# Kernel tuning notes

Measured on AMD Instinct MI355X. Metric: run time of the kernel, lower is better.

Reference implementation:

```python
import jax, jax.numpy as jnp
import numpy as np

N_QUBITS = 6
N_LAYERS = 3
FEATURE_DIM = 512
ENC_HIDDEN = max(32, N_QUBITS * 4)  # 32
HEAD_HIDDEN = 128
G, T = 54, 24
DIM = 2 ** N_QUBITS  # 64


def _ry_batched(angles):
    # angles: [B] -> batched RY matrices [B, 2, 2] (complex64)
    c = jnp.cos(angles * 0.5)
    s = jnp.sin(angles * 0.5)
    U = jnp.stack([jnp.stack([c, -s], -1), jnp.stack([s, c], -1)], -2)
    return U.astype(jnp.complex64)


def _rot(phi, theta, omega):
    # PennyLane Rot = RZ(omega) RY(theta) RZ(phi); returns [2, 2] complex64
    c = jnp.cos(theta * 0.5).astype(jnp.complex64)
    s = jnp.sin(theta * 0.5).astype(jnp.complex64)
    ep = jnp.exp(-0.5j * (phi + omega).astype(jnp.complex64))  # e^{-i(phi+omega)/2}
    em = jnp.exp(-0.5j * (phi - omega).astype(jnp.complex64))  # e^{-i(phi-omega)/2}
    u00 = ep * c
    u01 = -jnp.conj(em) * s
    u10 = em * s
    u11 = jnp.conj(ep) * c
    return jnp.stack([jnp.stack([u00, u01]), jnp.stack([u10, u11])])


def _apply_1q_batched(state, U, q):
    # state: [B, 2^n]; U: [B, 2, 2] (per-sample gate, e.g. data-encoding RY)
    B = state.shape[0]
    st = state.reshape(B, 2 ** q, 2, -1)
    st = jnp.einsum('bij,bljr->blir', U, st)
    return st.reshape(B, -1)


def _apply_1q(state, U, q):
    # state: [B, 2^n]; U: [2, 2] shared across batch (trainable Rot)
    B = state.shape[0]
    st = state.reshape(B, 2 ** q, 2, -1)
    st = jnp.einsum('ij,bljr->blir', U, st)
    return st.reshape(B, -1)


def _apply_cnot(state, c, t):
    # state: [B, 2^n]; flip target axis where control bit == 1
    B = state.shape[0]
    st = state.reshape((B,) + (2,) * N_QUBITS)
    ax_c, ax_t = 1 + c, 1 + t
    s0 = jnp.take(st, 0, axis=ax_c)
    s1 = jnp.take(st, 1, axis=ax_c)
    s1 = jnp.flip(s1, axis=ax_t if ax_t < ax_c else ax_t - 1)
    st = jnp.stack([s0, s1], axis=ax_c)
    return st.reshape(B, -1)


def _expvals_z(state):
    # <Z_q> for every qubit: [B, n]
    B = state.shape[0]
    probs = (state.real ** 2 + state.imag ** 2).reshape((B,) + (2,) * N_QUBITS)
    outs = []
    for q in range(N_QUBITS):
        axes = tuple(i for i in range(1, N_QUBITS + 1) if i != q + 1)
        p = probs.sum(axes)  # [B, 2]
        outs.append(p[:, 0] - p[:, 1])
    return jnp.stack(outs, -1)


def _circuit(angles, q_weights):
    # angles: [B, n_qubits] float32; q_weights: [L, n, 3]
    B = angles.shape[0]
    state = jnp.zeros((B, DIM), jnp.complex64).at[:, 0].set(1.0)
    for layer in range(N_LAYERS):
        # data_reuploading=True -> re-encode every layer
        for q in range(N_QUBITS):
            state = _apply_1q_batched(state, _ry_batched(angles[:, q]), q)
        for q in range(N_QUBITS):
            w = q_weights[layer, q]
            state = _apply_1q(state, _rot(w[0], w[1], w[2]), q)
        for q in range(0, N_QUBITS - 1, 2):
            state = _apply_cnot(state, q, q + 1)
        for q in range(1, N_QUBITS - 1, 2):
            state = _apply_cnot(state, q, q + 1)
        state = _apply_cnot(state, N_QUBITS - 1, 0)  # n_qubits > 2
    return _expvals_z(state)


def setup_inputs() -> dict:
    key = jax.random.key(0)
    ks = jax.random.split(key, 10)
    B = 32768
    return {
        'x': jax.random.normal(ks[0], (B, FEATURE_DIM), jnp.float32),
        'enc_w1': 0.05 * jax.random.normal(ks[1], (FEATURE_DIM, ENC_HIDDEN), jnp.float32),
        'enc_b1': jnp.zeros((ENC_HIDDEN,), jnp.float32),
        'enc_w2': 0.05 * jax.random.normal(ks[2], (ENC_HIDDEN, N_QUBITS), jnp.float32),
        'enc_b2': jnp.zeros((N_QUBITS,), jnp.float32),
        'q_weights': 0.01 * jax.random.normal(ks[3], (N_LAYERS, N_QUBITS, 3), jnp.float32),
        'head_w1': 0.1 * jax.random.normal(ks[4], (N_QUBITS, HEAD_HIDDEN), jnp.float32),
        'head_b1': jnp.zeros((HEAD_HIDDEN,), jnp.float32),
        'head_w2': 0.05 * jax.random.normal(ks[5], (HEAD_HIDDEN, G * T), jnp.float32),
        'head_b2': jnp.zeros((G * T,), jnp.float32),
    }


def reference(x, enc_w1, enc_b1, enc_w2, enc_b2, q_weights,
              head_w1, head_b1, head_w2, head_b2):
    # classical encoder -> angles [B, n_qubits]
    h = jnp.tanh(x @ enc_w1 + enc_b1)
    angles = h @ enc_w2 + enc_b2
    # batched state-vector PQC simulation
    z = _circuit(angles, q_weights).astype(jnp.float32)  # [B, n_qubits]
    # classical head (dropout is identity in eval)
    g = jax.nn.relu(z @ head_w1 + head_b1)
    logits = g @ head_w2 + head_b2
    return logits.reshape(-1, G, T)
```

## Files before the change

### kernel.cpp

```cpp
#include <hip/hip_runtime.h>

typedef __bf16 bf16x8 __attribute__((ext_vector_type(8)));
typedef float floatx4 __attribute__((ext_vector_type(4)));
typedef unsigned short ushort8 __attribute__((ext_vector_type(8)));

__device__ __forceinline__ unsigned short f2bf(float f) {
    unsigned u = __float_as_uint(f);
    u += 0x7fffu + ((u >> 16) & 1u);
    return (unsigned short)(u >> 16);
}

template <int ST>
__device__ __forceinline__ void apply_local(float* fr, float* fi,
    float m00r, float m00i, float m01r, float m01i,
    float m10r, float m10i, float m11r, float m11i) {
#pragma unroll
    for (int i = 0; i < 8; ++i) {
        if ((i & ST) == 0) {
            int i1 = i + ST;
            float r0 = fr[i], u0 = fi[i], r1 = fr[i1], u1 = fi[i1];
            fr[i]  = m00r * r0 - m00i * u0 + m01r * r1 - m01i * u1;
            fi[i]  = m00r * u0 + m00i * r0 + m01r * u1 + m01i * r1;
            fr[i1] = m10r * r0 - m10i * u0 + m11r * r1 - m11i * u1;
            fi[i1] = m10r * u0 + m10i * r0 + m11r * u1 + m11i * r1;
        }
    }
}

template <int XM>
__device__ __forceinline__ void apply_cross(float* fr, float* fi, bool hi,
    float m00r, float m00i, float m01r, float m01i,
    float m10r, float m10i, float m11r, float m11i) {
    float car = hi ? m10r : m00r, cai = hi ? m10i : m00i;
    float cbr = hi ? m11r : m01r, cbi = hi ? m11i : m01i;
#pragma unroll
    for (int j = 0; j < 8; ++j) {
        float mr = fr[j], mi = fi[j];
        float pr = __shfl_xor(mr, XM);
        float pi = __shfl_xor(mi, XM);
        float a0r = hi ? pr : mr, a0i = hi ? pi : mi;
        float a1r = hi ? mr : pr, a1i = hi ? mi : pi;
        fr[j] = car * a0r - cai * a0i + cbr * a1r - cbi * a1i;
        fi[j] = car * a0i + cai * a0r + cbr * a1i + cbi * a1r;
    }
}

#define SWAP2(a, b) { float _t = fr[a]; fr[a] = fr[b]; fr[b] = _t; \
                      _t = fi[a]; fi[a] = fi[b]; fi[b] = _t; }

__global__ __launch_bounds__(512) void prep_kernel(
    const float* __restrict__ hw2, unsigned short* __restrict__ w2t) {
    int t = blockIdx.x * 512 + threadIdx.x;
    int nn = t >> 4;
    int kc = (t & 15) * 8;
    if (nn < 1296) {
        ushort8 pk;
#pragma unroll
        for (int j = 0; j < 8; ++j) pk[j] = f2bf(hw2[(size_t)(kc + j) * 1296 + nn]);
        *(ushort8*)(w2t + (size_t)nn * 128 + kc) = pk;
    }
}

__global__ __launch_bounds__(512, 4) void front_kernel(
    const float* __restrict__ x, const float* __restrict__ w1,
    const float* __restrict__ b1, const float* __restrict__ w2,
    const float* __restrict__ b2, const float* __restrict__ qw,
    const float* __restrict__ hw1, const float* __restrict__ hb1,
    unsigned short* __restrict__ g) {

    __shared__ float part[8][64][33];
    __shared__ float umat_s[144];

    float (*hsh)[33] = part[0];
    float (*casa)[12] = (float (*)[12])part[1];

    int tid = threadIdx.x;

    if (tid < 18) {
        float phi = qw[tid * 3], theta = qw[tid * 3 + 1], omega = qw[tid * 3 + 2];
        float c = cosf(0.5f * theta), s = sinf(0.5f * theta);
        float po = 0.5f * (phi + omega), pm = 0.5f * (phi - omega);
        float epr = cosf(po), epi = -sinf(po);
        float emr = cosf(pm), emi = -sinf(pm);
        float* u = umat_s + tid * 8;
        u[0] = epr * c;  u[1] = epi * c;
        u[2] = -emr * s; u[3] = emi * s;
        u[4] = emr * s;  u[5] = emi * s;
        u[6] = epr * c;  u[7] = -epi * c;
    }

    int lane = tid & 63;
    int wave = tid >> 6;
    int swave = __builtin_amdgcn_readfirstlane(wave);
    size_t row = (size_t)blockIdx.x * 64 + lane;
    const float2* x2 = (const float2*)(x + row * 512 + swave * 64);
    const float* wseg = w1 + swave * 64 * 32;

    float acc[32];
#pragma unroll
    for (int j = 0; j < 32; ++j) acc[j] = 0.f;

#pragma clang loop unroll(disable)
    for (int k2 = 0; k2 < 32; ++k2) {
        float2 xv = x2[k2];
        const float* wr = wseg + k2 * 64;
#pragma unroll
        for (int j = 0; j < 32; ++j) acc[j] = fmaf(wr[j], xv.x, acc[j]);
#pragma unroll
        for (int j = 0; j < 32; ++j) acc[j] = fmaf(wr[32 + j], xv.y, acc[j]);
    }
#pragma unroll
    for (int j = 0; j < 32; ++j) part[wave][lane][j] = acc[j];
    __syncthreads();

    {
        int rl = tid & 63;
        int jg = (tid >> 6) * 4;
#pragma unroll
        for (int jj = 0; jj < 4; ++jj) {
            int j = jg + jj;
            float v = b1[j];
#pragma unroll
            for (int w = 0; w < 8; ++w) v += part[w][rl][j];
            hsh[rl][j] = tanhf(v);
        }
    }
    __syncthreads();

    if (tid < 384) {
        int row_a = tid & 63;
        int q = tid >> 6;
        float a = b2[q];
#pragma unroll
        for (int j = 0; j < 32; ++j) a = fmaf(hsh[row_a][j], w2[j * 6 + q], a);
        a *= 0.5f;
        casa[row_a][q * 2]     = cosf(a);
        casa[row_a][q * 2 + 1] = sinf(a);
    }
    __syncthreads();

    int s8 = lane & 7;
    int p = lane >> 3;
    int samp = wave * 8 + s8;
    bool pb4 = (p & 4) != 0, pb2 = (p & 2) != 0, pb1 = (p & 1) != 0;

    float ca[6], sa[6];
#pragma unroll
    for (int q = 0; q < 6; ++q) { ca[q] = casa[samp][q * 2]; sa[q] = casa[samp][q * 2 + 1]; }

    float fr[8], fi[8];
#pragma unroll
    for (int j = 0; j < 8; ++j) { fr[j] = 0.f; fi[j] = 0.f; }
    fr[0] = (p == 0) ? 1.f : 0.f;

#pragma clang loop unroll(disable)
    for (int layer = 0; layer < 3; ++layer) {
        const float* ub = umat_s + layer * 48;
#define MAT(Q)                                                            \
        const float* u = ub + (Q) * 8;                                    \
        float c = ca[Q], ss = sa[Q];                                      \
        float m00r = u[0] * c + u[2] * ss, m00i = u[1] * c + u[3] * ss;   \
        float m01r = u[2] * c - u[0] * ss, m01i = u[3] * c - u[1] * ss;   \
        float m10r = u[4] * c + u[6] * ss, m10i = u[5] * c + u[7] * ss;   \
        float m11r = u[6] * c - u[4] * ss, m11i = u[7] * c - u[5] * ss;
        { MAT(0) apply_cross<32>(fr, fi, pb4, m00r, m00i, m01r, m01i, m10r, m10i, m11r, m11i); }
        { MAT(1) apply_cross<16>(fr, fi, pb2, m00r, m00i, m01r, m01i, m10r, m10i, m11r, m11i); }
        { MAT(2) apply_cross<8>(fr, fi, pb1, m00r, m00i, m01r, m01i, m10r, m10i, m11r, m11i); }
        { MAT(3) apply_local<4>(fr, fi, m00r, m00i, m01r, m01i, m10r, m10i, m11r, m11i); }
        { MAT(4) apply_local<2>(fr, fi, m00r, m00i, m01r, m01i, m10r, m10i, m11r, m11i); }
        { MAT(5) apply_local<1>(fr, fi, m00r, m00i, m01r, m01i, m10r, m10i, m11r, m11i); }
#undef MAT
#pragma unroll
        for (int j = 0; j < 8; ++j) {
            float pr = __shfl_xor(fr[j], 16);
            float pi = __shfl_xor(fi[j], 16);
            fr[j] = pb4 ? pr : fr[j];
            fi[j] = pb4 ? pi : fi[j];
        }
        {
            float tr[8], ti[8];
#pragma unroll
            for (int j = 0; j < 8; ++j) { tr[j] = fr[j]; ti[j] = fi[j]; }
#pragma unroll
            for (int j = 0; j < 8; ++j) {
                fr[j] = pb1 ? tr[j ^ 4] : tr[j];
                fi[j] = pb1 ? ti[j ^ 4] : ti[j];
            }
        }
        SWAP2(2, 3) SWAP2(6, 7)
#pragma unroll
        for (int j = 0; j < 8; ++j) {
            float pr = __shfl_xor(fr[j], 8);
            float pi = __shfl_xor(fi[j], 8);
            fr[j] = pb2 ? pr : fr[j];
            fi[j] = pb2 ? pi : fi[j];
        }
        SWAP2(4, 6) SWAP2(5, 7)
#pragma unroll
        for (int j = 1; j < 8; j += 2) {
            fr[j] = __shfl_xor(fr[j], 32);
            fi[j] = __shfl_xor(fi[j], 32);
        }
    }

    float zt = 0.f, z3 = 0.f, z4 = 0.f, z5 = 0.f;
#pragma unroll
    for (int j = 0; j < 8; ++j) {
        float pp = fr[j] * fr[j] + fi[j] * fi[j];
        zt += pp;
        z3 += (j & 4) ? -pp : pp;
        z4 += (j & 2) ? -pp : pp;
        z5 += (j & 1) ? -pp : pp;
    }
    float zz[6];
    zz[0] = pb4 ? -zt : zt;
    zz[1] = pb2 ? -zt : zt;
    zz[2] = pb1 ? -zt : zt;
    zz[3] = z3; zz[4] = z4; zz[5] = z5;
#pragma unroll
    for (int q = 0; q < 6; ++q) {
        zz[q] += __shfl_xor(zz[q], 8);
        zz[q] += __shfl_xor(zz[q], 16);
        zz[q] += __shfl_xor(zz[q], 32);
    }

    {
        unsigned short* gp = g + ((size_t)blockIdx.x * 64 + samp) * 128 + p * 16;
#pragma unroll
        for (int half = 0; half < 2; ++half) {
            ushort8 pk;
#pragma unroll
            for (int jj = 0; jj < 8; ++jj) {
                int j = p * 16 + half * 8 + jj;
                float a = hb1[j];
#pragma unroll
                for (int q = 0; q < 6; ++q) a = fmaf(zz[q], hw1[q * 128 + j], a);
                a = fmaxf(a, 0.f);
                pk[jj] = f2bf(a);
            }
            *(ushort8*)(gp + half * 8) = pk;
        }
    }
}

__global__ __launch_bounds__(256) void head_gemm(
    const unsigned short* __restrict__ g, const unsigned short* __restrict__ w2t,
    const float* __restrict__ b2, float* __restrict__ out) {
    __shared__ unsigned short gl[16 * 128];

    int tid = threadIdx.x;
    int row0 = blockIdx.x * 16;

    {
        int r = tid >> 4;
        int u = tid & 15;
        ushort8 v = *(const ushort8*)(g + (size_t)(row0 + r) * 128 + u * 8);
        int us = u ^ (r & 7);
        *(ushort8*)(gl + r * 128 + us * 8) = v;
    }
    __syncthreads();

    int lane = tid & 63, wv = tid >> 6;
    int l15 = lane & 15, quad = lane >> 4;
    int a7 = l15 & 7;

    for (int n = wv; n < 27; n += 4) {
        int col0 = n * 48;
#pragma unroll
        for (int t = 0; t < 3; ++t) {
            const unsigned short* ap =
                w2t + (size_t)(col0 + t * 16 + l15) * 128 + quad * 8;

            floatx4 acc = (floatx4)0.f;
#pragma unroll
            for (int ks = 0; ks < 4; ++ks) {
                bf16x8 af = *(const bf16x8*)(ap + ks * 32);
                int u = (quad + 4 * ks) ^ a7;
                bf16x8 bf = *(const bf16x8*)(gl + l15 * 128 + u * 8);
                acc = __builtin_amdgcn_mfma_f32_16x16x32_bf16(af, bf, acc, 0, 0, 0);
            }

            const float* bb = b2 + col0 + t * 16 + quad * 4;
            floatx4 bias = { bb[0], bb[1], bb[2], bb[3] };
            floatx4 v = acc + bias;
            *(floatx4*)(out + (size_t)(row0 + l15) * 1296 + col0 + t * 16 + quad * 4) = v;
        }
    }
}

extern "C" void kernel_launch(void* const* d_in, const int* in_sizes, int n_in,
                              void* d_out, int out_size, void* d_ws, size_t ws_size,
                              hipStream_t stream) {
    const float* x   = (const float*)d_in[0];
    const float* ew1 = (const float*)d_in[1];
    const float* eb1 = (const float*)d_in[2];
    const float* ew2 = (const float*)d_in[3];
    const float* eb2 = (const float*)d_in[4];
    const float* qw  = (const float*)d_in[5];
    const float* hw1 = (const float*)d_in[6];
    const float* hb1 = (const float*)d_in[7];
    const float* hw2 = (const float*)d_in[8];
    const float* hb2 = (const float*)d_in[9];
    float* out = (float*)d_out;

    char* ws = (char*)d_ws;
    unsigned short* g   = (unsigned short*)(ws);
    unsigned short* w2t = (unsigned short*)(ws + 8388608);

    prep_kernel<<<dim3(41), dim3(512), 0, stream>>>(hw2, w2t);
    front_kernel<<<dim3(512), dim3(512), 0, stream>>>(
        x, ew1, eb1, ew2, eb2, qw, hw1, hb1, g);
    head_gemm<<<dim3(2048), dim3(256), 0, stream>>>(g, w2t, hb2, out);
}
```

Baseline: 370.9 us.

## Split front kernel into encoder and circuit kernels; fuse head layer-1 into GEMM

Splits the monolithic front kernel into an encoder kernel (256 threads, 4 waves each covering 128 input features) that writes angles, and a separate circuit kernel that computes cos/sin and runs the state-vector simulation, writing only 6 expectation values per sample. Rot-matrix setup moves into the prep kernel. The head's first layer (z @ hw1 + relu, bf16 pack) moves into the head GEMM prologue, so the 128-wide g intermediate is no longer written to or read from global memory. The cost is an extra kernel launch and small angles/z round trips, plus lower encoder parallelism per row.

```diff
diff --git a/kernel.cpp b/kernel.cpp
--- a/kernel.cpp
+++ b/kernel.cpp
@@ -49,8 +49,21 @@
                       _t = fi[a]; fi[a] = fi[b]; fi[b] = _t; }
 
 __global__ __launch_bounds__(512) void prep_kernel(
-    const float* __restrict__ hw2, unsigned short* __restrict__ w2t) {
+    const float* __restrict__ hw2, const float* __restrict__ qw,
+    unsigned short* __restrict__ w2t, float* __restrict__ umat) {
     int t = blockIdx.x * 512 + threadIdx.x;
+    if (t < 18) {
+        float phi = qw[t * 3], theta = qw[t * 3 + 1], omega = qw[t * 3 + 2];
+        float c = cosf(0.5f * theta), s = sinf(0.5f * theta);
+        float po = 0.5f * (phi + omega), pm = 0.5f * (phi - omega);
+        float epr = cosf(po), epi = -sinf(po);
+        float emr = cosf(pm), emi = -sinf(pm);
+        float* u = umat + t * 8;
+        u[0] = epr * c;  u[1] = epi * c;
+        u[2] = -emr * s; u[3] = emi * s;
+        u[4] = emr * s;  u[5] = emi * s;
+        u[6] = epr * c;  u[7] = -epi * c;
+    }
     int nn = t >> 4;
     int kc = (t & 15) * 8;
     if (nn < 1296) {
@@ -61,47 +74,25 @@
     }
 }
 
-__global__ __launch_bounds__(512, 4) void front_kernel(
+__global__ __launch_bounds__(256) void enc_kernel(
     const float* __restrict__ x, const float* __restrict__ w1,
     const float* __restrict__ b1, const float* __restrict__ w2,
-    const float* __restrict__ b2, const float* __restrict__ qw,
-    const float* __restrict__ hw1, const float* __restrict__ hb1,
-    unsigned short* __restrict__ g) {
-
-    __shared__ float part[8][64][33];
-    __shared__ float umat_s[144];
-
-    float (*hsh)[33] = part[0];
-    float (*casa)[12] = (float (*)[12])part[1];
-
-    int tid = threadIdx.x;
-
-    if (tid < 18) {
-        float phi = qw[tid * 3], theta = qw[tid * 3 + 1], omega = qw[tid * 3 + 2];
-        float c = cosf(0.5f * theta), s = sinf(0.5f * theta);
-        float po = 0.5f * (phi + omega), pm = 0.5f * (phi - omega);
-        float epr = cosf(po), epi = -sinf(po);
-        float emr = cosf(pm), emi = -sinf(pm);
-        float* u = umat_s + tid * 8;
-        u[0] = epr * c;  u[1] = epi * c;
-        u[2] = -emr * s; u[3] = emi * s;
-        u[4] = emr * s;  u[5] = emi * s;
-        u[6] = epr * c;  u[7] = -epi * c;
-    }
-
-    int lane = tid & 63;
-    int wave = tid >> 6;
+    const float* __restrict__ b2, float* __restrict__ angles) {
+    __shared__ float part[4][64][33];
+    __shared__ float hsh[64][33];
+    int lane = threadIdx.x & 63;
+    int wave = threadIdx.x >> 6;
     int swave = __builtin_amdgcn_readfirstlane(wave);
     size_t row = (size_t)blockIdx.x * 64 + lane;
-    const float2* x2 = (const float2*)(x + row * 512 + swave * 64);
-    const float* wseg = w1 + swave * 64 * 32;
+    const float2* x2 = (const float2*)(x + row * 512 + swave * 128);
+    const float* wseg = w1 + swave * 128 * 32;
 
     float acc[32];
 #pragma unroll
     for (int j = 0; j < 32; ++j) acc[j] = 0.f;
 
 #pragma clang loop unroll(disable)
-    for (int k2 = 0; k2 < 32; ++k2) {
+    for (int k2 = 0; k2 < 64; ++k2) {
         float2 xv = x2[k2];
         const float* wr = wseg + k2 * 64;
 #pragma unroll
@@ -113,40 +104,48 @@
     for (int j = 0; j < 32; ++j) part[wave][lane][j] = acc[j];
     __syncthreads();
 
-    {
-        int rl = tid & 63;
-        int jg = (tid >> 6) * 4;
-#pragma unroll
-        for (int jj = 0; jj < 4; ++jj) {
-            int j = jg + jj;
-            float v = b1[j];
-#pragma unroll
-            for (int w = 0; w < 8; ++w) v += part[w][rl][j];
-            hsh[rl][j] = tanhf(v);
-        }
+    int rl = threadIdx.x & 63;
+    int jg = (threadIdx.x >> 6) * 8;
+#pragma unroll
+    for (int jj = 0; jj < 8; ++jj) {
+        int j = jg + jj;
+        float v = part[0][rl][j] + part[1][rl][j] + part[2][rl][j] + part[3][rl][j] + b1[j];
+        hsh[rl][j] = tanhf(v);
     }
     __syncthreads();
 
-    if (tid < 384) {
-        int row_a = tid & 63;
-        int q = tid >> 6;
-        float a = b2[q];
-#pragma unroll
-        for (int j = 0; j < 32; ++j) a = fmaf(hsh[row_a][j], w2[j * 6 + q], a);
-        a *= 0.5f;
-        casa[row_a][q * 2]     = cosf(a);
-        casa[row_a][q * 2 + 1] = sinf(a);
-    }
-    __syncthreads();
-
+    if (threadIdx.x < 64) {
+        float h[32];
+#pragma unroll
+        for (int j = 0; j < 32; ++j) h[j] = hsh[threadIdx.x][j];
+#pragma unroll
+        for (int q = 0; q < 6; ++q) {
+            float a = b2[q];
+#pragma unroll
+            for (int j = 0; j < 32; ++j) a = fmaf(h[j], w2[j * 6 + q], a);
+            angles[((size_t)blockIdx.x * 64 + threadIdx.x) * 6 + q] = a;
+        }
+    }
+}
+
+__global__ __launch_bounds__(256) void circuit_kernel(
+    const float* __restrict__ angles, const float* __restrict__ umat,
+    float* __restrict__ z) {
+    int tid = threadIdx.x;
+    int lane = tid & 63;
+    int wv = tid >> 6;
     int s8 = lane & 7;
     int p = lane >> 3;
-    int samp = wave * 8 + s8;
+    int samp = blockIdx.x * 32 + wv * 8 + s8;
     bool pb4 = (p & 4) != 0, pb2 = (p & 2) != 0, pb1 = (p & 1) != 0;
 
     float ca[6], sa[6];
 #pragma unroll
-    for (int q = 0; q < 6; ++q) { ca[q] = casa[samp][q * 2]; sa[q] = casa[samp][q * 2 + 1]; }
+    for (int q = 0; q < 6; ++q) {
+        float a = 0.5f * angles[(size_t)samp * 6 + q];
+        ca[q] = cosf(a);
+        sa[q] = sinf(a);
+    }
 
     float fr[8], fi[8];
 #pragma unroll
@@ -155,7 +154,7 @@
 
 #pragma clang loop unroll(disable)
     for (int layer = 0; layer < 3; ++layer) {
-        const float* ub = umat_s + layer * 48;
+        const float* ub = umat + layer * 48;
 #define MAT(Q)                                                            \
         const float* u = ub + (Q) * 8;                                    \
         float c = ca[Q], ss = sa[Q];                                      \
@@ -223,40 +222,41 @@
         zz[q] += __shfl_xor(zz[q], 16);
         zz[q] += __shfl_xor(zz[q], 32);
     }
-
-    {
-        unsigned short* gp = g + ((size_t)blockIdx.x * 64 + samp) * 128 + p * 16;
-#pragma unroll
-        for (int half = 0; half < 2; ++half) {
-            ushort8 pk;
-#pragma unroll
-            for (int jj = 0; jj < 8; ++jj) {
-                int j = p * 16 + half * 8 + jj;
-                float a = hb1[j];
-#pragma unroll
-                for (int q = 0; q < 6; ++q) a = fmaf(zz[q], hw1[q * 128 + j], a);
-                a = fmaxf(a, 0.f);
-                pk[jj] = f2bf(a);
-            }
-            *(ushort8*)(gp + half * 8) = pk;
-        }
-    }
+    if (p < 6) z[(size_t)samp * 6 + p] = zz[p];
 }
 
 __global__ __launch_bounds__(256) void head_gemm(
-    const unsigned short* __restrict__ g, const unsigned short* __restrict__ w2t,
+    const float* __restrict__ z, const unsigned short* __restrict__ w2t,
+    const float* __restrict__ hw1, const float* __restrict__ hb1,
     const float* __restrict__ b2, float* __restrict__ out) {
     __shared__ unsigned short gl[16 * 128];
+    __shared__ float zsh[16][6];
 
     int tid = threadIdx.x;
     int row0 = blockIdx.x * 16;
+
+    if (tid < 96) zsh[tid / 6][tid % 6] = z[(size_t)row0 * 6 + tid];
+    __syncthreads();
 
     {
         int r = tid >> 4;
         int u = tid & 15;
-        ushort8 v = *(const ushort8*)(g + (size_t)(row0 + r) * 128 + u * 8);
+        int j0 = u * 8;
+        float zr[6];
+#pragma unroll
+        for (int q = 0; q < 6; ++q) zr[q] = zsh[r][q];
+        ushort8 pk;
+#pragma unroll
+        for (int jj = 0; jj < 8; ++jj) {
+            int j = j0 + jj;
+            float a = hb1[j];
+#pragma unroll
+            for (int q = 0; q < 6; ++q) a = fmaf(zr[q], hw1[q * 128 + j], a);
+            a = fmaxf(a, 0.f);
+            pk[jj] = f2bf(a);
+        }
         int us = u ^ (r & 7);
-        *(ushort8*)(gl + r * 128 + us * 8) = v;
+        *(ushort8*)(gl + r * 128 + us * 8) = pk;
     }
     __syncthreads();
 
@@ -304,11 +304,13 @@
     float* out = (float*)d_out;
 
     char* ws = (char*)d_ws;
-    unsigned short* g   = (unsigned short*)(ws);
-    unsigned short* w2t = (unsigned short*)(ws + 8388608);
-
-    prep_kernel<<<dim3(41), dim3(512), 0, stream>>>(hw2, w2t);
-    front_kernel<<<dim3(512), dim3(512), 0, stream>>>(
-        x, ew1, eb1, ew2, eb2, qw, hw1, hb1, g);
-    head_gemm<<<dim3(2048), dim3(256), 0, stream>>>(g, w2t, hb2, out);
-}
+    unsigned short* w2t = (unsigned short*)(ws);
+    float* umat   = (float*)(ws + 331776);
+    float* angles = (float*)(ws + 332352);
+    float* z      = (float*)(ws + 1118784);
+
+    prep_kernel<<<dim3(41), dim3(512), 0, stream>>>(hw2, qw, w2t, umat);
+    enc_kernel<<<dim3(512), dim3(256), 0, stream>>>(x, ew1, eb1, ew2, eb2, angles);
+    circuit_kernel<<<dim3(1024), dim3(256), 0, stream>>>(angles, umat, z);
+    head_gemm<<<dim3(2048), dim3(256), 0, stream>>>(z, w2t, hw1, hb1, hb2, out);
+}
```

After: 364.3 us. Within noise of the previous version (-1.8%).
